# Optimization experiments

Measured on AMD Instinct MI355X. Metric: run time of the kernel, lower is better.

The kernel has to match this reference:

```python
import jax, jax.numpy as jnp
import numpy as np

N = 200_000           # particles
E = 6_400_000         # neighbor pairs (~32 per particle)
SUPPORT = 0.05
EPS = SUPPORT ** 2 * 0.1
DELTA = 0.1
C0 = 10.0 * float(np.sqrt(2.0 * 9.81 * 0.3))
REST_DENSITY = 1000.0
_KC = 7.0 / float(np.pi)  # 2D Wendland C2 normalization


def kernel_gradient(q, dirs, h):
    # Wendland C2 (2D): W = C/h^2 (1-q)^4 (1+4q), q = r/h in [0,1]
    # dW/dr = C/h^3 * (-20 q (1-q)^3), directed along unit vector dirs
    dkdq = -20.0 * q * (1.0 - q) ** 3 * _KC
    return dirs * (dkdq / h ** 3)[:, None]


def setup_inputs() -> dict:
    key = jax.random.key(0)
    k = jax.random.split(key, 7)
    i = jnp.sort(jax.random.randint(k[0], (E,), 0, N))
    j = jax.random.randint(k[1], (E,), 0, N)
    fluidPosition = jax.random.uniform(k[2], (N, 2), dtype=jnp.float32)
    dx2 = (SUPPORT * 0.5) ** 2
    fluidVolume = dx2 * (1.0 + 0.01 * jax.random.normal(k[3], (N,), dtype=jnp.float32))
    fluidDensity = 0.95 + 0.1 * jax.random.uniform(k[4], (N,), dtype=jnp.float32)
    d = jax.random.normal(k[5], (E, 2), dtype=jnp.float32)
    distances = d / (jnp.linalg.norm(d, axis=1, keepdims=True) + 1e-8)  # unit directions
    radialDistances = jax.random.uniform(k[6], (E,), dtype=jnp.float32, minval=0.05, maxval=1.0)
    return {"fluidPosition": fluidPosition, "fluidVolume": fluidVolume,
            "fluidDensity": fluidDensity, "distances": distances,
            "radialDistances": radialDistances, "i": i, "j": j}


def reference(fluidPosition, fluidVolume, fluidDensity, distances, radialDistances, i, j):
    h = SUPPORT
    n = fluidDensity.shape[0]
    gradW = kernel_gradient(radialDistances, distances, h)          # [E,2]
    r_ba = -distances * (radialDistances * h)[:, None]              # [E,2] displacement
    Vj = fluidVolume[j]

    # --- normalization matrix: sum_j 2 Vj * outer(r_ba, gradW) ---
    term = jnp.einsum('nu,nv->nuv', r_ba, gradW) * (2.0 * Vj)[:, None, None]
    M = jax.ops.segment_sum(term, i, num_segments=n)                # [N,2,2]

    # --- pseudo-inverse + renormalized kernel gradient per edge ---
    Li = jnp.linalg.pinv(M)                                         # [N,2,2]
    grad = jnp.einsum('nuv,nv->nu', Li[i], gradW)                   # [E,2]
    dwij_mag = jnp.sum(jnp.abs(gradW), axis=1)                      # L1 norms
    norm_mag = jnp.sum(jnp.abs(grad), axis=1)
    change = jnp.abs(norm_mag - dwij_mag) / (dwij_mag + 1e-4 * h)
    grad = jnp.where((change < 0.1)[:, None], grad, gradW)

    # --- renormalized density gradient ---
    rho = fluidDensity * REST_DENSITY
    rho_ba = rho[j] - rho[i]
    gradRho = jax.ops.segment_sum((2.0 * rho_ba * Vj)[:, None] * grad, i, num_segments=n)

    # --- deltaSPH density diffusion ---
    rji2 = jnp.sum(r_ba * r_ba, axis=1) + EPS
    densityTerm = 0.5 * jnp.einsum('nu,nu->n', gradRho[i] + gradRho[j], r_ba)
    gradTerm = jnp.einsum('nu,nu->n', gradW, r_ba / rji2[:, None])
    prod = (rho_ba + densityTerm) * gradTerm
    return 2.0 * h * DELTA * C0 * jax.ops.segment_sum(prod * Vj, i, num_segments=n)
```

## Files before the change

kernel.cpp:

```cpp
#include <hip/hip_runtime.h>
#include <math.h>

#define WAVE   64
#define NPB    32
#define BLOCKT 256
#define SMAX   2

#define KC        2.2281692032865347f
#define H         0.05f
#define INV_H2    400.0f
#define INV_H3    8000.0f
#define EPS_REF   0.00025f
#define K_OUT     0.24261080f
#define REST_RHO  1000.0f

__device__ __forceinline__ float wendland_dkdq(float q) {
    float o = 1.f - q;
    return -20.f * q * o * o * o * KC;
}

template<int NV>
__device__ __forceinline__ void seg_reduce4(const int k[4], float v[4][NV], float* base) {
    const int lane = threadIdx.x & (WAVE - 1);
    const int k0 = k[0], k3 = k[3];
    const bool split = (k0 != k3);
    const int firstLen  = (k[1]==k0) ? ((k[2]==k0) ? ((k[3]==k0)?4:3) : 2) : 1;
    const int lastStart = (k[2]==k3) ? ((k[1]==k3) ? ((k[0]==k3)?0:1) : 2) : 3;

    float vin[NV], vfirst[NV];
#pragma unroll
    for (int c = 0; c < NV; ++c) {
        float s = v[3][c];
        if (lastStart <= 2) s += v[2][c];
        if (lastStart <= 1) s += v[1][c];
        if (lastStart == 0) s += v[0][c];
        vin[c] = s;
        float f = v[0][c];
        if (firstLen >= 2) f += v[1][c];
        if (firstLen >= 3) f += v[2][c];
        if (firstLen >= 4) f += v[3][c];
        vfirst[c] = f;
    }
#pragma unroll
    for (int idx = 1; idx <= 2; ++idx) {
        if (idx >= firstLen && idx < lastStart && k[idx] >= 0) {
#pragma unroll
            for (int c = 0; c < NV; ++c)
                atomicAdd(base + (size_t)k[idx] * NV + c, v[idx][c]);
        }
    }
    float S[NV];
#pragma unroll
    for (int c = 0; c < NV; ++c) S[c] = vin[c];
    const int klast = k3;
#pragma unroll
    for (int d = 1; d < WAVE; d <<= 1) {
        int okey = __shfl_up(klast, d, WAVE);
        float ov[NV];
#pragma unroll
        for (int c = 0; c < NV; ++c) ov[c] = __shfl_up(S[c], d, WAVE);
        if (lane >= d && okey == klast) {
#pragma unroll
            for (int c = 0; c < NV; ++c) S[c] += ov[c];
        }
    }
    const int prevk = __shfl_up(klast, 1, WAVE);
    float P[NV];
#pragma unroll
    for (int c = 0; c < NV; ++c) P[c] = __shfl_up(S[c], 1, WAVE);
    if (split && k0 >= 0) {
        const bool carry = (lane > 0 && prevk == k0);
#pragma unroll
        for (int c = 0; c < NV; ++c)
            atomicAdd(base + (size_t)k0 * NV + c, vfirst[c] + (carry ? P[c] : 0.f));
    }
    const int nk0 = __shfl_down(k0, 1, WAVE);
    const bool tail = (lane == WAVE - 1) || (nk0 != klast);
    if (tail && klast >= 0) {
#pragma unroll
        for (int c = 0; c < NV; ++c)
            atomicAdd(base + (size_t)klast * NV + c, S[c]);
    }
}

struct EW { int iv[4], jv[4]; float qv[4], dxv[4], dyv[4]; bool okv[4]; };

__device__ __forceinline__ void load_win(long e0, int beg, int end, int E,
        const int* __restrict__ ei, const int* __restrict__ ej,
        const float* __restrict__ qarr, const float2* __restrict__ dirs, EW& w) {
    if (e0 + 3 < (long)E) {
        int4   i4 = *(const int4*)(ei + e0);
        int4   j4 = *(const int4*)(ej + e0);
        float4 q4 = *(const float4*)(qarr + e0);
        float4 dA = *(const float4*)((const float*)dirs + 2 * e0);
        float4 dB = *(const float4*)((const float*)dirs + 2 * e0 + 4);
        w.iv[0]=i4.x; w.iv[1]=i4.y; w.iv[2]=i4.z; w.iv[3]=i4.w;
        w.jv[0]=j4.x; w.jv[1]=j4.y; w.jv[2]=j4.z; w.jv[3]=j4.w;
        w.qv[0]=q4.x; w.qv[1]=q4.y; w.qv[2]=q4.z; w.qv[3]=q4.w;
        w.dxv[0]=dA.x; w.dyv[0]=dA.y; w.dxv[1]=dA.z; w.dyv[1]=dA.w;
        w.dxv[2]=dB.x; w.dyv[2]=dB.y; w.dxv[3]=dB.z; w.dyv[3]=dB.w;
    } else {
#pragma unroll
        for (int u = 0; u < 4; ++u) {
            long e = e0 + u;
            if (e < (long)E) {
                w.iv[u] = ei[e]; w.jv[u] = ej[e]; w.qv[u] = qarr[e];
                float2 d = dirs[e]; w.dxv[u] = d.x; w.dyv[u] = d.y;
            } else { w.iv[u]=0; w.jv[u]=0; w.qv[u]=0.f; w.dxv[u]=0.f; w.dyv[u]=0.f; }
        }
    }
#pragma unroll
    for (int u = 0; u < 4; ++u) {
        long e = e0 + u;
        w.okv[u] = (e >= (long)beg) && (e < (long)end) && (e < (long)E);
    }
}

__global__ void k_prep(const int* __restrict__ ei, const float* __restrict__ vol,
                       const float* __restrict__ dens, int* __restrict__ rowptr,
                       float2* __restrict__ vd, int N, int E) {
    int e = blockIdx.x * blockDim.x + threadIdx.x;
    if (e <= E) {
        int prev = (e == 0) ? -1 : ei[e - 1];
        int cur  = (e == E) ? N  : ei[e];
        for (int t = prev + 1; t <= cur; ++t) rowptr[t] = e;
    }
    if (e < N) vd[e] = make_float2(vol[e], dens[e]);
}

__global__ __launch_bounds__(BLOCKT, 4)
void k_AC(const int* __restrict__ ei, const int* __restrict__ ej,
          const float* __restrict__ qarr, const float2* __restrict__ dirs,
          const float2* __restrict__ vd, const int* __restrict__ rowptr,
          float4* __restrict__ nd, int N, int E) {
    __shared__ float  Mld[NPB * 3];
    __shared__ float  Lild[NPB * 3];
    __shared__ float  gld[NPB * 2];
    __shared__ float2 vdl[NPB];
    const int tid = threadIdx.x;
    const int n0  = blockIdx.x * NPB;
    const int nHi = min(n0 + NPB, N);
    if (tid < NPB && n0 + tid < N) vdl[tid] = vd[n0 + tid];
    if (tid < NPB * 3) Mld[tid] = 0.f;
    if (tid < NPB * 2) gld[tid] = 0.f;
    __syncthreads();
    const int  beg  = rowptr[n0], end = rowptr[nHi];
    const long beg4 = (long)beg & ~3L;
    const int  waveBase = tid & ~(WAVE - 1);

    int   li_s[4 * SMAX];
    float w_s[4 * SMAX], dx_s[4 * SMAX], dy_s[4 * SMAX], val_s[4 * SMAX];
#pragma unroll
    for (int x = 0; x < 4 * SMAX; ++x) { li_s[x] = -1; w_s[x]=dx_s[x]=dy_s[x]=val_s[x]=0.f; }

#pragma unroll
    for (int c = 0; c < SMAX; ++c) {
        long ebw = beg4 + ((long)c * BLOCKT + waveBase) * 4;
        if (ebw < (long)end) {
            long e0 = beg4 + ((long)c * BLOCKT + tid) * 4;
            EW wd; load_win(e0, beg, end, E, ei, ej, qarr, dirs, wd);
            int k[4]; float v[4][3];
#pragma unroll
            for (int u = 0; u < 4; ++u) {
                k[u] = -1; v[u][0] = v[u][1] = v[u][2] = 0.f;
                if (wd.okv[u]) {
                    int li = wd.iv[u] - n0;
                    float q = wd.qv[u], dx = wd.dxv[u], dy = wd.dyv[u];
                    float2 vdj = vd[wd.jv[u]];
                    float wq = wendland_dkdq(q);
                    float s = -2.f * vdj.x * q * wq * INV_H2;
                    k[u] = li;
                    v[u][0] = s * dx * dx; v[u][1] = s * dx * dy; v[u][2] = s * dy * dy;
                    li_s[c*4+u] = li; w_s[c*4+u] = wq * INV_H3;
                    dx_s[c*4+u] = dx; dy_s[c*4+u] = dy;
                    val_s[c*4+u] = 2.f * REST_RHO * (vdj.y - vdl[li].y) * vdj.x;
                }
            }
            seg_reduce4<3>(k, v, Mld);
        }
    }
    for (int c = SMAX; ; ++c) {
        long ebw = beg4 + ((long)c * BLOCKT + waveBase) * 4;
        if (ebw >= (long)end) break;
        long e0 = beg4 + ((long)c * BLOCKT + tid) * 4;
        EW wd; load_win(e0, beg, end, E, ei, ej, qarr, dirs, wd);
        int k[4]; float v[4][3];
#pragma unroll
        for (int u = 0; u < 4; ++u) {
            k[u] = -1; v[u][0] = v[u][1] = v[u][2] = 0.f;
            if (wd.okv[u]) {
                int li = wd.iv[u] - n0;
                float q = wd.qv[u], dx = wd.dxv[u], dy = wd.dyv[u];
                float2 vdj = vd[wd.jv[u]];
                float s = -2.f * vdj.x * q * wendland_dkdq(q) * INV_H2;
                k[u] = li;
                v[u][0] = s * dx * dx; v[u][1] = s * dx * dy; v[u][2] = s * dy * dy;
            }
        }
        seg_reduce4<3>(k, v, Mld);
    }
    __syncthreads();

    if (tid < NPB) {
        float a = Mld[3*tid], b = Mld[3*tid+1], cc = Mld[3*tid+2];
        float half_tr   = 0.5f * (a + cc);
        float half_diff = 0.5f * (a - cc);
        float disc = sqrtf(half_diff * half_diff + b * b);
        float l1 = half_tr + disc, l2 = half_tr - disc;
        float smax = fmaxf(fabsf(l1), fabsf(l2));
        float cutoff = 2.3841858e-6f * smax;
        float i00 = 0.f, i01 = 0.f, i11 = 0.f;
        if (fabsf(l2) > cutoff) {
            float inv = 1.0f / (a * cc - b * b);
            i00 =  cc * inv; i01 = -b * inv; i11 = a * inv;
        } else if (fabsf(l1) > cutoff) {
            float vax = b,       vay = l1 - a;
            float vbx = l1 - cc, vby = b;
            float na = vax*vax + vay*vay, nb = vbx*vbx + vby*vby;
            float vx, vy, n2;
            if (nb >= na) { vx = vbx; vy = vby; n2 = nb; }
            else          { vx = vax; vy = vay; n2 = na; }
            float inv = 1.0f / (l1 * n2);
            i00 = vx*vx*inv; i01 = vx*vy*inv; i11 = vy*vy*inv;
        }
        Lild[3*tid] = i00; Lild[3*tid+1] = i01; Lild[3*tid+2] = i11;
    }
    __syncthreads();

#pragma unroll
    for (int c = 0; c < SMAX; ++c) {
        long ebw = beg4 + ((long)c * BLOCKT + waveBase) * 4;
        if (ebw < (long)end) {
            int k[4]; float v[4][2];
#pragma unroll
            for (int u = 0; u < 4; ++u) {
                int li = li_s[c*4+u];
                k[u] = li; v[u][0] = v[u][1] = 0.f;
                if (li >= 0) {
                    float w = w_s[c*4+u], dx = dx_s[c*4+u], dy = dy_s[c*4+u];
                    float gwx = dx * w, gwy = dy * w;
                    float L0 = Lild[3*li], L1 = Lild[3*li+1], L2v = Lild[3*li+2];
                    float gx = L0 * gwx + L1 * gwy;
                    float gy = L1 * gwx + L2v * gwy;
                    float dm = fabsf(gwx) + fabsf(gwy);
                    float nm = fabsf(gx) + fabsf(gy);
                    float change = fabsf(nm - dm) / (dm + 1e-4f * H);
                    if (!(change < 0.1f)) { gx = gwx; gy = gwy; }
                    v[u][0] = val_s[c*4+u] * gx;
                    v[u][1] = val_s[c*4+u] * gy;
                }
            }
            seg_reduce4<2>(k, v, gld);
        }
    }
    for (int c = SMAX; ; ++c) {
        long ebw = beg4 + ((long)c * BLOCKT + waveBase) * 4;
        if (ebw >= (long)end) break;
        long e0 = beg4 + ((long)c * BLOCKT + tid) * 4;
        EW wd; load_win(e0, beg, end, E, ei, ej, qarr, dirs, wd);
        int k[4]; float v[4][2];
#pragma unroll
        for (int u = 0; u < 4; ++u) {
            k[u] = -1; v[u][0] = v[u][1] = 0.f;
            if (wd.okv[u]) {
                int li = wd.iv[u] - n0;
                float q = wd.qv[u], dx = wd.dxv[u], dy = wd.dyv[u];
                float2 vdj = vd[wd.jv[u]];
                float w = wendland_dkdq(q) * INV_H3;
                float gwx = dx * w, gwy = dy * w;
                float L0 = Lild[3*li], L1 = Lild[3*li+1], L2v = Lild[3*li+2];
                float gx = L0 * gwx + L1 * gwy;
                float gy = L1 * gwx + L2v * gwy;
                float dm = fabsf(gwx) + fabsf(gwy);
                float nm = fabsf(gx) + fabsf(gy);
                float change = fabsf(nm - dm) / (dm + 1e-4f * H);
                if (!(change < 0.1f)) { gx = gwx; gy = gwy; }
                float val = 2.f * REST_RHO * (vdj.y - vdl[li].y) * vdj.x;
                k[u] = li; v[u][0] = val * gx; v[u][1] = val * gy;
            }
        }
        seg_reduce4<2>(k, v, gld);
    }
    __syncthreads();
    if (tid < NPB && n0 + tid < N)
        nd[n0 + tid] = make_float4(vdl[tid].x, vdl[tid].y, gld[2*tid], gld[2*tid+1]);
}

__global__ __launch_bounds__(BLOCKT, 4)
void k_D(const int* __restrict__ ei, const int* __restrict__ ej,
         const float* __restrict__ qarr, const float2* __restrict__ dirs,
         const float4* __restrict__ nd, const int* __restrict__ rowptr,
         float* __restrict__ out, int N, int E) {
    __shared__ float4 ndl[NPB];
    __shared__ float  outl[NPB];
    const int tid = threadIdx.x;
    const int n0  = blockIdx.x * NPB;
    const int nHi = min(n0 + NPB, N);
    if (tid < NPB && n0 + tid < N) ndl[tid] = nd[n0 + tid];
    if (tid < NPB) outl[tid] = 0.f;
    __syncthreads();
    const int  beg  = rowptr[n0], end = rowptr[nHi];
    const long beg4 = (long)beg & ~3L;
    const int  waveBase = tid & ~(WAVE - 1);

    for (int c = 0; ; ++c) {
        long ebw = beg4 + ((long)c * BLOCKT + waveBase) * 4;
        if (ebw >= (long)end) break;
        long e0 = beg4 + ((long)c * BLOCKT + tid) * 4;
        EW wd; load_win(e0, beg, end, E, ei, ej, qarr, dirs, wd);
        float4 ndj[4];
#pragma unroll
        for (int u = 0; u < 4; ++u) ndj[u] = wd.okv[u] ? nd[wd.jv[u]] : make_float4(0,0,0,0);
        int k[4]; float v[4][1];
#pragma unroll
        for (int u = 0; u < 4; ++u) {
            k[u] = -1; v[u][0] = 0.f;
            if (wd.okv[u]) {
                int li = wd.iv[u] - n0;
                float4 ndi = ndl[li];
                float q = wd.qv[u], dx = wd.dxv[u], dy = wd.dyv[u];
                float w = wendland_dkdq(q) * INV_H3;
                float gwx = dx * w, gwy = dy * w;
                float rx = -dx * q * H, ry = -dy * q * H;
                float rji2 = rx * rx + ry * ry + EPS_REF;
                float gradTerm = (gwx * rx + gwy * ry) / rji2;
                float densityTerm = 0.5f * ((ndi.z + ndj[u].z) * rx + (ndi.w + ndj[u].w) * ry);
                float rho_ba = REST_RHO * (ndj[u].y - ndi.y);
                k[u] = li;
                v[u][0] = (rho_ba + densityTerm) * gradTerm * ndj[u].x;
            }
        }
        seg_reduce4<1>(k, v, outl);
    }
    __syncthreads();
    if (tid < NPB && n0 + tid < N) out[n0 + tid] = outl[tid] * K_OUT;
}

extern "C" void kernel_launch(void* const* d_in, const int* in_sizes, int n_in,
                              void* d_out, int out_size, void* d_ws, size_t ws_size,
                              hipStream_t stream) {
    const float*  vol  = (const float*)d_in[1];
    const float*  dens = (const float*)d_in[2];
    const float2* dirs = (const float2*)d_in[3];
    const float*  qarr = (const float*)d_in[4];
    const int*    ei   = (const int*)d_in[5];
    const int*    ej   = (const int*)d_in[6];
    const int N = in_sizes[1];
    const int E = in_sizes[4];

    char*   p      = (char*)d_ws;
    int*    rowptr = (int*)p;      p += (((size_t)(N + 1) * 4) + 15) & ~(size_t)15;
    float2* vd     = (float2*)p;   p += (size_t)N * sizeof(float2);
    float4* nd     = (float4*)p;
    float*  out    = (float*)d_out;

    const int tb = 256;
    const int gP = (E + 1 + tb - 1) / tb;
    const int gB = (N + NPB - 1) / NPB;

    k_prep<<<gP, tb, 0, stream>>>(ei, vol, dens, rowptr, vd, N, E);
    k_AC  <<<gB, BLOCKT, 0, stream>>>(ei, ej, qarr, dirs, vd, rowptr, nd, N, E);
    k_D   <<<gB, BLOCKT, 0, stream>>>(ei, ej, qarr, dirs, nd, rowptr, out, N, E);
}
```

Before: 247.2 us.

## Split density-diffusion sum algebraically and stash per-edge half-precision coefficients for final pass

The final pass is expanded algebraically. The parts that do not depend on the density gradient (rho_ba*gradTerm and r*gradTerm moments) are accumulated in the first pass as three extra per-node sums. The only part left is per-edge gradRho[j]·c, with c stored in fp16 per edge, so the last kernel reads just j, a 4-byte coefficient and g2[j] instead of the full edge data and a float4 gather. Node indices are now recovered by binary search over a shared rowptr slice instead of loading the i array. The trade-offs are extra atomics and registers in the first pass, an E-sized write of the coefficients, and fp16 rounding error in the density term.

```diff
diff --git a/kernel.cpp b/kernel.cpp
--- a/kernel.cpp
+++ b/kernel.cpp
@@ -1,4 +1,5 @@
 #include <hip/hip_runtime.h>
+#include <hip/hip_fp16.h>
 #include <math.h>
 
 #define WAVE   64
@@ -17,6 +18,17 @@
 __device__ __forceinline__ float wendland_dkdq(float q) {
     float o = 1.f - q;
     return -20.f * q * o * o * o * KC;
+}
+
+union H2F { __half2 h; float f; };
+__device__ __forceinline__ float   h2_as_f(__half2 h) { H2F u; u.h = h; return u.f; }
+__device__ __forceinline__ __half2 f_as_h2(float f)   { H2F u; u.f = f; return u.h; }
+
+__device__ __forceinline__ int li_search(const int* rp, int e) {
+    int lo = 0;
+#pragma unroll
+    for (int s = NPB / 2; s >= 1; s >>= 1) lo += (rp[lo + s] <= e) ? s : 0;
+    return lo;
 }
 
 template<int NV>
@@ -83,18 +95,16 @@
     }
 }
 
-struct EW { int iv[4], jv[4]; float qv[4], dxv[4], dyv[4]; bool okv[4]; };
+struct EW { int jv[4]; float qv[4], dxv[4], dyv[4]; bool okv[4]; };
 
 __device__ __forceinline__ void load_win(long e0, int beg, int end, int E,
-        const int* __restrict__ ei, const int* __restrict__ ej,
-        const float* __restrict__ qarr, const float2* __restrict__ dirs, EW& w) {
+        const int* __restrict__ ej, const float* __restrict__ qarr,
+        const float2* __restrict__ dirs, EW& w) {
     if (e0 + 3 < (long)E) {
-        int4   i4 = *(const int4*)(ei + e0);
         int4   j4 = *(const int4*)(ej + e0);
         float4 q4 = *(const float4*)(qarr + e0);
         float4 dA = *(const float4*)((const float*)dirs + 2 * e0);
         float4 dB = *(const float4*)((const float*)dirs + 2 * e0 + 4);
-        w.iv[0]=i4.x; w.iv[1]=i4.y; w.iv[2]=i4.z; w.iv[3]=i4.w;
         w.jv[0]=j4.x; w.jv[1]=j4.y; w.jv[2]=j4.z; w.jv[3]=j4.w;
         w.qv[0]=q4.x; w.qv[1]=q4.y; w.qv[2]=q4.z; w.qv[3]=q4.w;
         w.dxv[0]=dA.x; w.dyv[0]=dA.y; w.dxv[1]=dA.z; w.dyv[1]=dA.w;
@@ -104,15 +114,15 @@
         for (int u = 0; u < 4; ++u) {
             long e = e0 + u;
             if (e < (long)E) {
-                w.iv[u] = ei[e]; w.jv[u] = ej[e]; w.qv[u] = qarr[e];
+                w.jv[u] = ej[e]; w.qv[u] = qarr[e];
                 float2 d = dirs[e]; w.dxv[u] = d.x; w.dyv[u] = d.y;
-            } else { w.iv[u]=0; w.jv[u]=0; w.qv[u]=0.f; w.dxv[u]=0.f; w.dyv[u]=0.f; }
+            } else { w.jv[u]=0; w.qv[u]=0.f; w.dxv[u]=0.f; w.dyv[u]=0.f; }
         }
     }
 #pragma unroll
     for (int u = 0; u < 4; ++u) {
         long e = e0 + u;
-        w.okv[u] = (e >= (long)beg) && (e < (long)end) && (e < (long)E);
+        w.okv[u] = (e >= (long)beg) && (e < (long)end);
     }
 }
 
@@ -129,22 +139,24 @@
 }
 
 __global__ __launch_bounds__(BLOCKT, 4)
-void k_AC(const int* __restrict__ ei, const int* __restrict__ ej,
-          const float* __restrict__ qarr, const float2* __restrict__ dirs,
-          const float2* __restrict__ vd, const int* __restrict__ rowptr,
-          float4* __restrict__ nd, int N, int E) {
-    __shared__ float  Mld[NPB * 3];
+void k_AC(const int* __restrict__ ej, const float* __restrict__ qarr,
+          const float2* __restrict__ dirs, const float2* __restrict__ vd,
+          const int* __restrict__ rowptr, __half2* __restrict__ cst,
+          float2* __restrict__ g2, float* __restrict__ outp, int N, int E) {
+    __shared__ int    rp[NPB + 1];
+    __shared__ float  acc6[NPB * 6];
     __shared__ float  Lild[NPB * 3];
     __shared__ float  gld[NPB * 2];
     __shared__ float2 vdl[NPB];
     const int tid = threadIdx.x;
     const int n0  = blockIdx.x * NPB;
     const int nHi = min(n0 + NPB, N);
+    if (tid <= NPB) rp[tid] = rowptr[min(n0 + tid, nHi)];
     if (tid < NPB && n0 + tid < N) vdl[tid] = vd[n0 + tid];
-    if (tid < NPB * 3) Mld[tid] = 0.f;
+    if (tid < NPB * 6) acc6[tid] = 0.f;
     if (tid < NPB * 2) gld[tid] = 0.f;
     __syncthreads();
-    const int  beg  = rowptr[n0], end = rowptr[nHi];
+    const int  beg = rp[0], end = rp[NPB];
     const long beg4 = (long)beg & ~3L;
     const int  waveBase = tid & ~(WAVE - 1);
 
@@ -158,51 +170,79 @@
         long ebw = beg4 + ((long)c * BLOCKT + waveBase) * 4;
         if (ebw < (long)end) {
             long e0 = beg4 + ((long)c * BLOCKT + tid) * 4;
-            EW wd; load_win(e0, beg, end, E, ei, ej, qarr, dirs, wd);
-            int k[4]; float v[4][3];
+            EW wd; load_win(e0, beg, end, E, ej, qarr, dirs, wd);
+            const bool all4 = wd.okv[0] && wd.okv[1] && wd.okv[2] && wd.okv[3];
+            float4 cpack;
+            int k[4]; float v[4][6];
 #pragma unroll
             for (int u = 0; u < 4; ++u) {
-                k[u] = -1; v[u][0] = v[u][1] = v[u][2] = 0.f;
+                k[u] = -1;
+#pragma unroll
+                for (int c2 = 0; c2 < 6; ++c2) v[u][c2] = 0.f;
                 if (wd.okv[u]) {
-                    int li = wd.iv[u] - n0;
+                    int li = li_search(rp, (int)(e0 + u));
                     float q = wd.qv[u], dx = wd.dxv[u], dy = wd.dyv[u];
                     float2 vdj = vd[wd.jv[u]];
                     float wq = wendland_dkdq(q);
                     float s = -2.f * vdj.x * q * wq * INV_H2;
+                    float w = wq * INV_H3;
+                    float gwx = dx * w, gwy = dy * w;
+                    float rx = -dx * q * H, ry = -dy * q * H;
+                    float rji2 = rx * rx + ry * ry + EPS_REF;
+                    float gT = (gwx * rx + gwy * ry) / rji2;
+                    float gv = gT * vdj.x;
+                    float rho_ba = REST_RHO * (vdj.y - vdl[li].y);
                     k[u] = li;
                     v[u][0] = s * dx * dx; v[u][1] = s * dx * dy; v[u][2] = s * dy * dy;
-                    li_s[c*4+u] = li; w_s[c*4+u] = wq * INV_H3;
+                    v[u][3] = rho_ba * gv; v[u][4] = rx * gv;    v[u][5] = ry * gv;
+                    __half2 cp = __floats2half2_rn(0.5f * rx * gv, 0.5f * ry * gv);
+                    if (all4) (&cpack.x)[u] = h2_as_f(cp);
+                    else      cst[e0 + u] = cp;
+                    li_s[c*4+u] = li; w_s[c*4+u] = w;
                     dx_s[c*4+u] = dx; dy_s[c*4+u] = dy;
-                    val_s[c*4+u] = 2.f * REST_RHO * (vdj.y - vdl[li].y) * vdj.x;
+                    val_s[c*4+u] = 2.f * rho_ba * vdj.x;
                 }
             }
-            seg_reduce4<3>(k, v, Mld);
+            if (all4) ((float4*)cst)[e0 >> 2] = cpack;
+            seg_reduce4<6>(k, v, acc6);
         }
     }
     for (int c = SMAX; ; ++c) {
         long ebw = beg4 + ((long)c * BLOCKT + waveBase) * 4;
         if (ebw >= (long)end) break;
         long e0 = beg4 + ((long)c * BLOCKT + tid) * 4;
-        EW wd; load_win(e0, beg, end, E, ei, ej, qarr, dirs, wd);
-        int k[4]; float v[4][3];
+        EW wd; load_win(e0, beg, end, E, ej, qarr, dirs, wd);
+        int k[4]; float v[4][6];
 #pragma unroll
         for (int u = 0; u < 4; ++u) {
-            k[u] = -1; v[u][0] = v[u][1] = v[u][2] = 0.f;
+            k[u] = -1;
+#pragma unroll
+            for (int c2 = 0; c2 < 6; ++c2) v[u][c2] = 0.f;
             if (wd.okv[u]) {
-                int li = wd.iv[u] - n0;
+                int li = li_search(rp, (int)(e0 + u));
                 float q = wd.qv[u], dx = wd.dxv[u], dy = wd.dyv[u];
                 float2 vdj = vd[wd.jv[u]];
-                float s = -2.f * vdj.x * q * wendland_dkdq(q) * INV_H2;
+                float wq = wendland_dkdq(q);
+                float s = -2.f * vdj.x * q * wq * INV_H2;
+                float w = wq * INV_H3;
+                float gwx = dx * w, gwy = dy * w;
+                float rx = -dx * q * H, ry = -dy * q * H;
+                float rji2 = rx * rx + ry * ry + EPS_REF;
+                float gT = (gwx * rx + gwy * ry) / rji2;
+                float gv = gT * vdj.x;
+                float rho_ba = REST_RHO * (vdj.y - vdl[li].y);
                 k[u] = li;
                 v[u][0] = s * dx * dx; v[u][1] = s * dx * dy; v[u][2] = s * dy * dy;
-            }
-        }
-        seg_reduce4<3>(k, v, Mld);
+                v[u][3] = rho_ba * gv; v[u][4] = rx * gv;    v[u][5] = ry * gv;
+                cst[e0 + u] = __floats2half2_rn(0.5f * rx * gv, 0.5f * ry * gv);
+            }
+        }
+        seg_reduce4<6>(k, v, acc6);
     }
     __syncthreads();
 
     if (tid < NPB) {
-        float a = Mld[3*tid], b = Mld[3*tid+1], cc = Mld[3*tid+2];
+        float a = acc6[6*tid], b = acc6[6*tid+1], cc = acc6[6*tid+2];
         float half_tr   = 0.5f * (a + cc);
         float half_diff = 0.5f * (a - cc);
         float disc = sqrtf(half_diff * half_diff + b * b);
@@ -257,13 +297,13 @@
         long ebw = beg4 + ((long)c * BLOCKT + waveBase) * 4;
         if (ebw >= (long)end) break;
         long e0 = beg4 + ((long)c * BLOCKT + tid) * 4;
-        EW wd; load_win(e0, beg, end, E, ei, ej, qarr, dirs, wd);
+        EW wd; load_win(e0, beg, end, E, ej, qarr, dirs, wd);
         int k[4]; float v[4][2];
 #pragma unroll
         for (int u = 0; u < 4; ++u) {
             k[u] = -1; v[u][0] = v[u][1] = 0.f;
             if (wd.okv[u]) {
-                int li = wd.iv[u] - n0;
+                int li = li_search(rp, (int)(e0 + u));
                 float q = wd.qv[u], dx = wd.dxv[u], dy = wd.dyv[u];
                 float2 vdj = vd[wd.jv[u]];
                 float w = wendland_dkdq(q) * INV_H3;
@@ -282,24 +322,26 @@
         seg_reduce4<2>(k, v, gld);
     }
     __syncthreads();
-    if (tid < NPB && n0 + tid < N)
-        nd[n0 + tid] = make_float4(vdl[tid].x, vdl[tid].y, gld[2*tid], gld[2*tid+1]);
+    if (tid < NPB && n0 + tid < N) {
+        float gx = gld[2*tid], gy = gld[2*tid+1];
+        g2[n0 + tid]   = make_float2(gx, gy);
+        outp[n0 + tid] = acc6[6*tid+3] + 0.5f * (gx * acc6[6*tid+4] + gy * acc6[6*tid+5]);
+    }
 }
 
 __global__ __launch_bounds__(BLOCKT, 4)
-void k_D(const int* __restrict__ ei, const int* __restrict__ ej,
-         const float* __restrict__ qarr, const float2* __restrict__ dirs,
-         const float4* __restrict__ nd, const int* __restrict__ rowptr,
-         float* __restrict__ out, int N, int E) {
-    __shared__ float4 ndl[NPB];
-    __shared__ float  outl[NPB];
+void k_D(const int* __restrict__ ej, const __half2* __restrict__ cst,
+         const float2* __restrict__ g2, const float* __restrict__ outp,
+         const int* __restrict__ rowptr, float* __restrict__ out, int N, int E) {
+    __shared__ int   rp[NPB + 1];
+    __shared__ float outl[NPB];
     const int tid = threadIdx.x;
     const int n0  = blockIdx.x * NPB;
     const int nHi = min(n0 + NPB, N);
-    if (tid < NPB && n0 + tid < N) ndl[tid] = nd[n0 + tid];
+    if (tid <= NPB) rp[tid] = rowptr[min(n0 + tid, nHi)];
     if (tid < NPB) outl[tid] = 0.f;
     __syncthreads();
-    const int  beg  = rowptr[n0], end = rowptr[nHi];
+    const int  beg = rp[0], end = rp[NPB];
     const long beg4 = (long)beg & ~3L;
     const int  waveBase = tid & ~(WAVE - 1);
 
@@ -307,33 +349,42 @@
         long ebw = beg4 + ((long)c * BLOCKT + waveBase) * 4;
         if (ebw >= (long)end) break;
         long e0 = beg4 + ((long)c * BLOCKT + tid) * 4;
-        EW wd; load_win(e0, beg, end, E, ei, ej, qarr, dirs, wd);
-        float4 ndj[4];
-#pragma unroll
-        for (int u = 0; u < 4; ++u) ndj[u] = wd.okv[u] ? nd[wd.jv[u]] : make_float4(0,0,0,0);
+        int jv[4]; float cv[4]; bool okv[4];
+        if (e0 + 3 < (long)E) {
+            int4   j4 = *(const int4*)(ej + e0);
+            float4 c4 = ((const float4*)cst)[e0 >> 2];
+            jv[0]=j4.x; jv[1]=j4.y; jv[2]=j4.z; jv[3]=j4.w;
+            cv[0]=c4.x; cv[1]=c4.y; cv[2]=c4.z; cv[3]=c4.w;
+        } else {
+#pragma unroll
+            for (int u = 0; u < 4; ++u) {
+                long e = e0 + u;
+                if (e < (long)E) { jv[u] = ej[e]; cv[u] = h2_as_f(cst[e]); }
+                else             { jv[u] = 0;     cv[u] = 0.f; }
+            }
+        }
+#pragma unroll
+        for (int u = 0; u < 4; ++u) {
+            long e = e0 + u;
+            okv[u] = (e >= (long)beg) && (e < (long)end);
+        }
         int k[4]; float v[4][1];
 #pragma unroll
         for (int u = 0; u < 4; ++u) {
             k[u] = -1; v[u][0] = 0.f;
-            if (wd.okv[u]) {
-                int li = wd.iv[u] - n0;
-                float4 ndi = ndl[li];
-                float q = wd.qv[u], dx = wd.dxv[u], dy = wd.dyv[u];
-                float w = wendland_dkdq(q) * INV_H3;
-                float gwx = dx * w, gwy = dy * w;
-                float rx = -dx * q * H, ry = -dy * q * H;
-                float rji2 = rx * rx + ry * ry + EPS_REF;
-                float gradTerm = (gwx * rx + gwy * ry) / rji2;
-                float densityTerm = 0.5f * ((ndi.z + ndj[u].z) * rx + (ndi.w + ndj[u].w) * ry);
-                float rho_ba = REST_RHO * (ndj[u].y - ndi.y);
+            if (okv[u]) {
+                int li = li_search(rp, (int)(e0 + u));
+                float2 gj = g2[jv[u]];
+                __half2 ch = f_as_h2(cv[u]);
                 k[u] = li;
-                v[u][0] = (rho_ba + densityTerm) * gradTerm * ndj[u].x;
+                v[u][0] = gj.x * __low2float(ch) + gj.y * __high2float(ch);
             }
         }
         seg_reduce4<1>(k, v, outl);
     }
     __syncthreads();
-    if (tid < NPB && n0 + tid < N) out[n0 + tid] = outl[tid] * K_OUT;
+    if (tid < NPB && n0 + tid < N)
+        out[n0 + tid] = K_OUT * (outp[n0 + tid] + outl[tid]);
 }
 
 extern "C" void kernel_launch(void* const* d_in, const int* in_sizes, int n_in,
@@ -348,17 +399,21 @@
     const int N = in_sizes[1];
     const int E = in_sizes[4];
 
-    char*   p      = (char*)d_ws;
-    int*    rowptr = (int*)p;      p += (((size_t)(N + 1) * 4) + 15) & ~(size_t)15;
-    float2* vd     = (float2*)p;   p += (size_t)N * sizeof(float2);
-    float4* nd     = (float4*)p;
-    float*  out    = (float*)d_out;
+    size_t off = 0;
+    auto alloc = [&](size_t bytes) { void* r = (char*)d_ws + off;
+                                     off = (off + bytes + 15) & ~(size_t)15; return r; };
+    int*     rowptr = (int*)    alloc((size_t)(N + 1) * 4);
+    float2*  vd     = (float2*) alloc((size_t)N * 8);
+    float2*  g2     = (float2*) alloc((size_t)N * 8);
+    float*   outp   = (float*)  alloc((size_t)N * 4);
+    __half2* cst    = (__half2*)alloc((size_t)E * 4);
+    float*   out    = (float*)d_out;
 
     const int tb = 256;
     const int gP = (E + 1 + tb - 1) / tb;
     const int gB = (N + NPB - 1) / NPB;
 
     k_prep<<<gP, tb, 0, stream>>>(ei, vol, dens, rowptr, vd, N, E);
-    k_AC  <<<gB, BLOCKT, 0, stream>>>(ei, ej, qarr, dirs, vd, rowptr, nd, N, E);
-    k_D   <<<gB, BLOCKT, 0, stream>>>(ei, ej, qarr, dirs, nd, rowptr, out, N, E);
-}
+    k_AC  <<<gB, BLOCKT, 0, stream>>>(ej, qarr, dirs, vd, rowptr, cst, g2, outp, N, E);
+    k_D   <<<gB, BLOCKT, 0, stream>>>(ej, cst, g2, outp, rowptr, out, N, E);
+}
```

Measured after the change: 245.5 us. Within noise of the previous version (-0.7%).
